# Performance work log

Hardware: AMD Instinct MI355X
Metric: run time of the kernel (lower is better)

The kernel has to match this reference:

```python
import jax, jax.numpy as jnp
import numpy as np

B = 2097152  # batch of complex chemical-potential samples


def _dense(h, Wr, Wi, br, bi):
    # complex dense: h @ (Wr + i Wi) + (br + i bi)
    return h @ jax.lax.complex(Wr, Wi) + jax.lax.complex(br, bi)


def _pade(h, ar, ai, qr, qi):
    # degree-4/4 Pade rational activation, coefficients shared across units
    # P(h) = a0 + a1 h + a2 h^2 + a3 h^3 + a4 h^4
    # Q(h) = 1  + q1 h + q2 h^2 + q3 h^3 + q4 h^4   (safe=False)
    a = jax.lax.complex(ar, ai)  # [5]
    q = jax.lax.complex(qr, qi)  # [4]
    num = a[4]
    for j in (3, 2, 1, 0):
        num = num * h + a[j]
    den = q[3]
    for k in (2, 1, 0):
        den = den * h + q[k]
    den = den * h + jnp.asarray(1.0, h.dtype)
    return num / den


def setup_inputs() -> dict:
    key = jax.random.key(0)
    ks = jax.random.split(key, 24)
    f32 = jnp.float32

    def rn(k, shape, scale):
        return jax.random.normal(k, shape, f32) * scale

    # input: (Re mu, Im mu) pairs, kept small so exp() stays well-scaled
    x = rn(ks[0], (B, 2), 0.3)

    inp = {"x": x}
    # complex dense layers 1->8->4->1 (glorot-ish scale on each part)
    inp["W1r"] = rn(ks[1], (1, 8), 0.5); inp["W1i"] = rn(ks[2], (1, 8), 0.5)
    inp["b1r"] = rn(ks[3], (8,), 0.1);   inp["b1i"] = rn(ks[4], (8,), 0.1)
    inp["W2r"] = rn(ks[5], (8, 4), 0.3); inp["W2i"] = rn(ks[6], (8, 4), 0.3)
    inp["b2r"] = rn(ks[7], (4,), 0.1);   inp["b2i"] = rn(ks[8], (4,), 0.1)
    inp["W3r"] = rn(ks[9], (4, 1), 0.4); inp["W3i"] = rn(ks[10], (4, 1), 0.4)
    inp["b3r"] = rn(ks[11], (1,), 0.1);  inp["b3i"] = rn(ks[12], (1,), 0.1)
    # Pade coefficients: numerator initialized near identity (get_alphas),
    # denominator near 1 (small q), perturbed by noise
    ident = jnp.asarray([0.0, 1.0, 0.0, 0.0, 0.0], f32)
    inp["a1r"] = ident + rn(ks[13], (5,), 0.05); inp["a1i"] = rn(ks[14], (5,), 0.05)
    inp["q1r"] = rn(ks[15], (4,), 0.05);         inp["q1i"] = rn(ks[16], (4,), 0.05)
    inp["a2r"] = ident + rn(ks[17], (5,), 0.05); inp["a2i"] = rn(ks[18], (5,), 0.05)
    inp["q2r"] = rn(ks[19], (4,), 0.05);         inp["q2i"] = rn(ks[20], (4,), 0.05)
    return inp


def reference(x, W1r, W1i, b1r, b1i, a1r, a1i, q1r, q1i,
              W2r, W2i, b2r, b2i, a2r, a2i, q2r, q2i,
              W3r, W3i, b3r, b3i):
    # CFugacityCoV: mu -> fugacity z = exp(mu)
    z = jnp.exp(jax.lax.complex(x[:, :1], x[:, 1:]))        # [B,1] complex64
    h = _pade(_dense(z, W1r, W1i, b1r, b1i), a1r, a1i, q1r, q1i)  # [B,8]
    h = _pade(_dense(h, W2r, W2i, b2r, b2i), a2r, a2i, q2r, q2i)  # [B,4]
    o = _dense(h, W3r, W3i, b3r, b3i)                        # [B,1] complex
    # CSplitReIm
    return jnp.concatenate([jnp.real(o), jnp.imag(o)], axis=-1)  # [B,2] f32
```

## Files before the change

### kernel.cpp

```cpp
#include <hip/hip_runtime.h>

struct Cx { float r, i; };

__device__ __forceinline__ Cx cmadd(Cx a, Cx h, Cx c) {
    Cx o;
    o.r = fmaf(a.r, h.r, fmaf(-a.i, h.i, c.r));
    o.i = fmaf(a.r, h.i, fmaf( a.i, h.r, c.i));
    return o;
}

__device__ __forceinline__ Cx pade(Cx h, const Cx A[5], const Cx Q[4]) {
    Cx num = A[4];
    num = cmadd(num, h, A[3]);
    num = cmadd(num, h, A[2]);
    num = cmadd(num, h, A[1]);
    num = cmadd(num, h, A[0]);
    Cx den = Q[3];
    den = cmadd(den, h, Q[2]);
    den = cmadd(den, h, Q[1]);
    den = cmadd(den, h, Q[0]);
    den = cmadd(den, h, Cx{1.0f, 0.0f});
    float inv = __builtin_amdgcn_rcpf(fmaf(den.r, den.r, den.i * den.i));
    Cx o;
    o.r = fmaf(num.r, den.r,  num.i * den.i) * inv;
    o.i = fmaf(num.i, den.r, -num.r * den.i) * inv;
    return o;
}

__global__ __launch_bounds__(256, 8) void pade_model_kernel(
    const float2* __restrict__ x,
    const float* __restrict__ W1r, const float* __restrict__ W1i,
    const float* __restrict__ b1r, const float* __restrict__ b1i,
    const float* __restrict__ W2r, const float* __restrict__ W2i,
    const float* __restrict__ b2r, const float* __restrict__ b2i,
    const float* __restrict__ W3r, const float* __restrict__ W3i,
    const float* __restrict__ b3r, const float* __restrict__ b3i,
    const float* __restrict__ a1r, const float* __restrict__ a1i,
    const float* __restrict__ q1r, const float* __restrict__ q1i,
    const float* __restrict__ a2r, const float* __restrict__ a2i,
    const float* __restrict__ q2r, const float* __restrict__ q2i,
    float2* __restrict__ out)
{
    __shared__ float2 lds[57];
    int t = threadIdx.x;
    if (t < 57) {
        float r, i;
        if      (t <  8) { r = W1r[t];      i = W1i[t]; }
        else if (t < 16) { r = b1r[t - 8];  i = b1i[t - 8]; }
        else if (t < 48) { r = W2r[t - 16]; i = W2i[t - 16]; }
        else if (t < 52) { r = b2r[t - 48]; i = b2i[t - 48]; }
        else if (t < 56) { r = W3r[t - 52]; i = W3i[t - 52]; }
        else             { r = b3r[0];      i = b3i[0]; }
        lds[t] = {r, i};
    }
    __syncthreads();

    Cx A1[5], Q1[4], A2[5], Q2[4];
    #pragma unroll
    for (int j = 0; j < 5; ++j) { A1[j] = {a1r[j], a1i[j]}; A2[j] = {a2r[j], a2i[j]}; }
    #pragma unroll
    for (int j = 0; j < 4; ++j) { Q1[j] = {q1r[j], q1i[j]}; Q2[j] = {q2r[j], q2i[j]}; }

    int idx = blockIdx.x * blockDim.x + t;

    float2 xv = x[idx];
    float er = __expf(xv.x);
    Cx z{er * __cosf(xv.y), er * __sinf(xv.y)};

    auto L = [&](int k) -> Cx { float2 v = lds[k]; return {v.x, v.y}; };

    Cx h2[4];
    #pragma unroll
    for (int k = 0; k < 4; ++k) h2[k] = L(48 + k);

    #pragma unroll
    for (int j = 0; j < 8; ++j) {
        Cx u = pade(cmadd(z, L(j), L(8 + j)), A1, Q1);
        #pragma unroll
        for (int k = 0; k < 4; ++k)
            h2[k] = cmadd(u, L(16 + j * 4 + k), h2[k]);
    }

    #pragma unroll
    for (int k = 0; k < 4; ++k) h2[k] = pade(h2[k], A2, Q2);

    Cx o = L(56);
    #pragma unroll
    for (int k = 0; k < 4; ++k) o = cmadd(h2[k], L(52 + k), o);

    out[idx] = {o.r, o.i};
}

extern "C" void kernel_launch(void* const* d_in, const int* in_sizes, int n_in,
                              void* d_out, int out_size, void* d_ws, size_t ws_size,
                              hipStream_t stream) {
    const float2* x  = (const float2*)d_in[0];
    const float* W1r = (const float*)d_in[1];
    const float* W1i = (const float*)d_in[2];
    const float* b1r = (const float*)d_in[3];
    const float* b1i = (const float*)d_in[4];
    const float* W2r = (const float*)d_in[5];
    const float* W2i = (const float*)d_in[6];
    const float* b2r = (const float*)d_in[7];
    const float* b2i = (const float*)d_in[8];
    const float* W3r = (const float*)d_in[9];
    const float* W3i = (const float*)d_in[10];
    const float* b3r = (const float*)d_in[11];
    const float* b3i = (const float*)d_in[12];
    const float* a1r = (const float*)d_in[13];
    const float* a1i = (const float*)d_in[14];
    const float* q1r = (const float*)d_in[15];
    const float* q1i = (const float*)d_in[16];
    const float* a2r = (const float*)d_in[17];
    const float* a2i = (const float*)d_in[18];
    const float* q2r = (const float*)d_in[19];
    const float* q2i = (const float*)d_in[20];

    int n = in_sizes[0] / 2;
    float2* out = (float2*)d_out;

    dim3 block(256);
    dim3 grid(n / 256);
    pade_model_kernel<<<grid, block, 0, stream>>>(
        x, W1r, W1i, b1r, b1i, W2r, W2i, b2r, b2i, W3r, W3i, b3r, b3i,
        a1r, a1i, q1r, q1i, a2r, a2i, q2r, q2i, out);
}
```

Measured before the change: 33.78 us.

## Process four samples per thread with float4 loads and stores

Each thread now handles four samples: two float4 loads cover two pairs of adjacent samples, one pair offset by a half-grid stride, and results are written back as two float4 stores. The grid shrinks fourfold, so the per-block LDS weight staging, barrier and Pade coefficient loads are amortised over more work, and there is more independent ILP per thread. Launch bounds drop from 8 to 2 blocks per SM, letting the compiler use more registers for the four unrolled forward passes, at the cost of fewer resident waves.

```diff
diff --git a/kernel.cpp b/kernel.cpp
--- a/kernel.cpp
+++ b/kernel.cpp
@@ -27,8 +27,8 @@
     return o;
 }
 
-__global__ __launch_bounds__(256, 8) void pade_model_kernel(
-    const float2* __restrict__ x,
+__global__ __launch_bounds__(256, 2) void pade_model_kernel(
+    const float4* __restrict__ x4,
     const float* __restrict__ W1r, const float* __restrict__ W1i,
     const float* __restrict__ b1r, const float* __restrict__ b1i,
     const float* __restrict__ W2r, const float* __restrict__ W2i,
@@ -39,7 +39,7 @@
     const float* __restrict__ q1r, const float* __restrict__ q1i,
     const float* __restrict__ a2r, const float* __restrict__ a2i,
     const float* __restrict__ q2r, const float* __restrict__ q2i,
-    float2* __restrict__ out)
+    float4* __restrict__ out4, int nthreads)
 {
     __shared__ float2 lds[57];
     int t = threadIdx.x;
@@ -61,40 +61,47 @@
     #pragma unroll
     for (int j = 0; j < 4; ++j) { Q1[j] = {q1r[j], q1i[j]}; Q2[j] = {q2r[j], q2i[j]}; }
 
-    int idx = blockIdx.x * blockDim.x + t;
-
-    float2 xv = x[idx];
-    float er = __expf(xv.x);
-    Cx z{er * __cosf(xv.y), er * __sinf(xv.y)};
-
     auto L = [&](int k) -> Cx { float2 v = lds[k]; return {v.x, v.y}; };
 
-    Cx h2[4];
-    #pragma unroll
-    for (int k = 0; k < 4; ++k) h2[k] = L(48 + k);
+    auto fwd = [&](float xr, float xi) -> Cx {
+        float er = __expf(xr);
+        Cx z{er * __cosf(xi), er * __sinf(xi)};
+        Cx h2[4];
+        #pragma unroll
+        for (int k = 0; k < 4; ++k) h2[k] = L(48 + k);
+        #pragma unroll
+        for (int j = 0; j < 8; ++j) {
+            Cx u = pade(cmadd(z, L(j), L(8 + j)), A1, Q1);
+            #pragma unroll
+            for (int k = 0; k < 4; ++k)
+                h2[k] = cmadd(u, L(16 + j * 4 + k), h2[k]);
+        }
+        #pragma unroll
+        for (int k = 0; k < 4; ++k) h2[k] = pade(h2[k], A2, Q2);
+        Cx o = L(56);
+        #pragma unroll
+        for (int k = 0; k < 4; ++k) o = cmadd(h2[k], L(52 + k), o);
+        return o;
+    };
 
-    #pragma unroll
-    for (int j = 0; j < 8; ++j) {
-        Cx u = pade(cmadd(z, L(j), L(8 + j)), A1, Q1);
-        #pragma unroll
-        for (int k = 0; k < 4; ++k)
-            h2[k] = cmadd(u, L(16 + j * 4 + k), h2[k]);
-    }
+    int i0 = blockIdx.x * blockDim.x + t;
+    int i1 = i0 + nthreads;
+    float4 v0 = x4[i0];
+    float4 v1 = x4[i1];
 
-    #pragma unroll
-    for (int k = 0; k < 4; ++k) h2[k] = pade(h2[k], A2, Q2);
+    Cx o0 = fwd(v0.x, v0.y);
+    Cx o1 = fwd(v0.z, v0.w);
+    Cx o2 = fwd(v1.x, v1.y);
+    Cx o3 = fwd(v1.z, v1.w);
 
-    Cx o = L(56);
-    #pragma unroll
-    for (int k = 0; k < 4; ++k) o = cmadd(h2[k], L(52 + k), o);
-
-    out[idx] = {o.r, o.i};
+    out4[i0] = {o0.r, o0.i, o1.r, o1.i};
+    out4[i1] = {o2.r, o2.i, o3.r, o3.i};
 }
 
 extern "C" void kernel_launch(void* const* d_in, const int* in_sizes, int n_in,
                               void* d_out, int out_size, void* d_ws, size_t ws_size,
                               hipStream_t stream) {
-    const float2* x  = (const float2*)d_in[0];
+    const float4* x4 = (const float4*)d_in[0];
     const float* W1r = (const float*)d_in[1];
     const float* W1i = (const float*)d_in[2];
     const float* b1r = (const float*)d_in[3];
@@ -117,11 +124,12 @@
     const float* q2i = (const float*)d_in[20];
 
     int n = in_sizes[0] / 2;
-    float2* out = (float2*)d_out;
+    int nthreads = n / 4;
+    float4* out4 = (float4*)d_out;
 
     dim3 block(256);
-    dim3 grid(n / 256);
+    dim3 grid(nthreads / 256);
     pade_model_kernel<<<grid, block, 0, stream>>>(
-        x, W1r, W1i, b1r, b1i, W2r, W2i, b2r, b2i, W3r, W3i, b3r, b3i,
-        a1r, a1i, q1r, q1i, a2r, a2i, q2r, q2i, out);
+        x4, W1r, W1i, b1r, b1i, W2r, W2i, b2r, b2i, W3r, W3i, b3r, b3i,
+        a1r, a1i, q1r, q1i, a2r, a2i, q2r, q2i, out4, nthreads);
 }
```

After: 33.84 us. No clear change (+0.2%).
